# Optimization experiments

Measured on AMD Instinct MI355X. Metric: run time of the kernel, lower is better.

## Reference

```python
import jax, jax.numpy as jnp
import numpy as np

EMBED_DIM = 1024
NUM_HEADS = 16
HEAD_DIM = EMBED_DIM // NUM_HEADS
BSZ, SEQ = 2, 2048


def setup_inputs() -> dict:
    key = jax.random.key(0)
    ks = jax.random.split(key, 7)
    s = 0.02  # keep logits in a sane range
    return {
        "hidden_states": jax.random.normal(ks[0], (BSZ, SEQ, EMBED_DIM), jnp.float32),
        "attention_mask": jnp.zeros((1, 1, SEQ, SEQ), jnp.float32),
        "q_w": jax.random.normal(ks[1], (2 * EMBED_DIM, EMBED_DIM), jnp.float32) * s,
        "q_b": jnp.zeros((2 * EMBED_DIM,), jnp.float32),
        "k_w": jax.random.normal(ks[2], (EMBED_DIM, EMBED_DIM), jnp.float32) * s,
        "k_b": jnp.zeros((EMBED_DIM,), jnp.float32),
        "v_w": jax.random.normal(ks[3], (EMBED_DIM, EMBED_DIM), jnp.float32) * s,
        "v_b": jnp.zeros((EMBED_DIM,), jnp.float32),
        "o_w": jax.random.normal(ks[4], (EMBED_DIM, EMBED_DIM), jnp.float32) * s,
        "o_b": jnp.zeros((EMBED_DIM,), jnp.float32),
    }


def reference(hidden_states, attention_mask, q_w, q_b, k_w, k_b, v_w, v_b, o_w, o_b):
    bsz, seq, _ = hidden_states.shape
    h, d = NUM_HEADS, HEAD_DIM
    inv_sqrt_d = 1.0 / np.sqrt(d).astype(np.float32)

    qg = hidden_states @ q_w.T + q_b                      # [b, s, 2*h*d]
    q, gate_logits = jnp.split(qg, [h * d], axis=-1)       # elementwise gate
    k = hidden_states @ k_w.T + k_b
    v = hidden_states @ v_w.T + v_b

    q = q.reshape(bsz, seq, h, d).transpose(0, 2, 1, 3)    # [b, h, s, d]
    k = k.reshape(bsz, seq, h, d).transpose(0, 2, 1, 3)
    v = v.reshape(bsz, seq, h, d).transpose(0, 2, 1, 3)

    scores = jnp.einsum("bhqd,bhkd->bhqk", q, k) * inv_sqrt_d
    scores = scores + attention_mask
    weights = jax.nn.softmax(scores, axis=-1)
    attn = jnp.einsum("bhqk,bhkd->bhqd", weights, v)       # [b, h, s, d]

    gate = jax.nn.sigmoid(gate_logits.reshape(bsz, seq, h, d).transpose(0, 2, 1, 3))
    attn = attn * gate

    attn = attn.transpose(0, 2, 1, 3).reshape(bsz, seq, h * d)
    return attn @ o_w.T + o_b
```

## Files before the change

### kernel.cpp

```cpp
#include <hip/hip_runtime.h>
#include <cstdint>
#include <cstddef>

#define AS1 __attribute__((address_space(1)))
#define AS3 __attribute__((address_space(3)))

typedef __bf16 bf16x8 __attribute__((ext_vector_type(8)));
typedef __bf16 bf16x4 __attribute__((ext_vector_type(4)));
typedef float  f32x4  __attribute__((ext_vector_type(4)));
typedef float  f32x16 __attribute__((ext_vector_type(16)));
typedef unsigned int u32x4 __attribute__((ext_vector_type(4)));

#define MFMA_BF16(a, b, c) __builtin_amdgcn_mfma_f32_16x16x32_bf16((a), (b), (c), 0, 0, 0)
#define MFMA32(a, b, c)    __builtin_amdgcn_mfma_f32_32x32x16_bf16((a), (b), (c), 0, 0, 0)

__device__ __forceinline__ void gload16(const __bf16* g, __bf16* l) {
  __builtin_amdgcn_global_load_lds((AS1 void*)(uintptr_t)g, (AS3 void*)l, 16, 0, 0);
}

__device__ __forceinline__ unsigned int cvtpk_bf16(float lo, float hi) {
  unsigned int r;
  asm("v_cvt_pk_bf16_f32 %0, %1, %2" : "=v"(r) : "v"(lo), "v"(hi));
  return r;
}

__device__ __forceinline__ void permswap(unsigned int& a, unsigned int& b) {
  asm volatile("v_permlane32_swap_b32 %0, %1" : "+v"(a), "+v"(b));
}

__device__ __forceinline__ float exp2_fast(float x) {
  float r;
  asm("v_exp_f32 %0, %1" : "=v"(r) : "v"(x));
  return r;
}

#define LOG2E 1.4426950408889634f

__global__ void cvt_all_kernel(
    const float* __restrict__ hs, const float* __restrict__ qw, const float* __restrict__ kw,
    const float* __restrict__ vw, const float* __restrict__ ow,
    __bf16* __restrict__ Xb, __bf16* __restrict__ qwb, __bf16* __restrict__ kwb,
    __bf16* __restrict__ vwb, __bf16* __restrict__ owb,
    const unsigned long long* __restrict__ mask, int* __restrict__ flag)
{
  const int gid = blockIdx.x * blockDim.x + threadIdx.x;
  const int stride = gridDim.x * blockDim.x;
  for (int i = gid; i < 1179648; i += stride) {
    const float* s; __bf16* d; int o;
    if (i < 524288)       { s = hs; d = Xb;  o = i; }
    else if (i < 786432)  { s = qw; d = qwb; o = i - 524288; }
    else if (i < 917504)  { s = kw; d = kwb; o = i - 786432; }
    else if (i < 1048576) { s = vw; d = vwb; o = i - 917504; }
    else                  { s = ow; d = owb; o = i - 1048576; }
    const float4* p = (const float4*)(s + (size_t)o * 8);
    float4 a = p[0], b = p[1];
    bf16x8 v;
    v[0] = (__bf16)a.x; v[1] = (__bf16)a.y; v[2] = (__bf16)a.z; v[3] = (__bf16)a.w;
    v[4] = (__bf16)b.x; v[5] = (__bf16)b.y; v[6] = (__bf16)b.z; v[7] = (__bf16)b.w;
    *(bf16x8*)(d + (size_t)o * 8) = v;
  }
  bool nz = false;
  for (int i = gid; i < 2097152; i += stride) nz |= (mask[i] != 0ull);
  if (nz) atomicOr(flag, 1);
}

__global__ __launch_bounds__(256) void proj_kernel(
    const __bf16* __restrict__ X,
    const __bf16* __restrict__ qw, const float* __restrict__ qb,
    const __bf16* __restrict__ kw, const float* __restrict__ kb,
    const __bf16* __restrict__ vw, const float* __restrict__ vb,
    __bf16* __restrict__ Qo, __bf16* __restrict__ Ko,
    __bf16* __restrict__ VTo, __bf16* __restrict__ Go)
{
  __shared__ __bf16 As[2][128][64];
  __shared__ __bf16 Bs[2][128][64];

  const int bid = blockIdx.x;
  const int r = bid >> 3;
  const int ntile = (bid & 7) * 4 + (r >> 5);
  const int mtile = r & 31;
  const int m0 = mtile * 128;
  const int n0 = ntile * 128;

  const __bf16* W; const float* bias; int nb;
  if (n0 < 2048)      { W = qw; bias = qb; nb = n0; }
  else if (n0 < 3072) { W = kw; bias = kb; nb = n0 - 2048; }
  else                { W = vw; bias = vb; nb = n0 - 3072; }

  const int tid = threadIdx.x;
  const int wv = tid >> 6, ln = tid & 63;
  const int wr = wv >> 1, wc = wv & 1;
  const int qr = ln & 15, qg = ln >> 4;
  const int lrow = ln >> 3, lcol = (ln & 7) * 8;

  f32x4 acc[4][4];
#pragma unroll
  for (int m = 0; m < 4; ++m)
#pragma unroll
    for (int n = 0; n < 4; ++n) acc[m][n] = 0.f;

  __bf16 (*Asc)[64] = As[0], (*Asn)[64] = As[1];
  __bf16 (*Bsc)[64] = Bs[0], (*Bsn)[64] = Bs[1];

#pragma unroll
  for (int i = 0; i < 4; ++i) {
    const int rb = i * 32 + wv * 8;
    gload16(X + (size_t)(m0 + rb + lrow) * 1024 + lcol, &Asc[rb][0]);
    gload16(W + (size_t)(nb + rb + lrow) * 1024 + lcol, &Bsc[rb][0]);
  }
  __syncthreads();

  for (int t = 0; t < 16; ++t) {
    if (t < 15) {
      const int k0 = (t + 1) * 64;
#pragma unroll
      for (int i = 0; i < 4; ++i) {
        const int rb = i * 32 + wv * 8;
        gload16(X + (size_t)(m0 + rb + lrow) * 1024 + k0 + lcol, &Asn[rb][0]);
        gload16(W + (size_t)(nb + rb + lrow) * 1024 + k0 + lcol, &Bsn[rb][0]);
      }
    }
#pragma unroll
    for (int kk = 0; kk < 2; ++kk) {
      bf16x8 af[4], bfv[4];
#pragma unroll
      for (int m = 0; m < 4; ++m) af[m] = *(const bf16x8*)&Asc[wr * 64 + m * 16 + qr][kk * 32 + qg * 8];
#pragma unroll
      for (int n = 0; n < 4; ++n) bfv[n] = *(const bf16x8*)&Bsc[wc * 64 + n * 16 + qr][kk * 32 + qg * 8];
#pragma unroll
      for (int m = 0; m < 4; ++m)
#pragma unroll
        for (int n = 0; n < 4; ++n) acc[m][n] = MFMA_BF16(af[m], bfv[n], acc[m][n]);
    }
    __syncthreads();
    __bf16 (*ta)[64] = Asc; Asc = Asn; Asn = ta;
    __bf16 (*tb)[64] = Bsc; Bsc = Bsn; Bsn = tb;
  }

#pragma unroll
  for (int m = 0; m < 4; ++m) {
    const int gm0 = m0 + wr * 64 + m * 16 + qg * 4;
    const int b = gm0 >> 11;
    const int s = gm0 & 2047;
#pragma unroll
    for (int n = 0; n < 4; ++n) {
      const int nl = wc * 64 + n * 16 + qr;
      const float bb = bias[nb + nl];
      if (n0 < 1024) {
        const int col = n0 + nl, hh = col >> 6, dd = col & 63;
        __bf16* dst = Qo + ((size_t)((b << 4) + hh)) * 131072 + (size_t)s * 64 + dd;
#pragma unroll
        for (int rr = 0; rr < 4; ++rr) dst[(size_t)rr * 64] = (__bf16)((acc[m][n][rr] + bb) * (0.125f * LOG2E));
      } else if (n0 < 2048) {
        const int j = n0 - 1024 + nl;
        __bf16* dst = Go + (size_t)gm0 * 1024 + j;
#pragma unroll
        for (int rr = 0; rr < 4; ++rr) {
          const float v = acc[m][n][rr] + bb;
          dst[(size_t)rr * 1024] = (__bf16)(1.f / (1.f + __expf(-v)));
        }
      } else if (n0 < 3072) {
        const int j = n0 - 2048 + nl, hh = j >> 6, dd = j & 63;
        __bf16* dst = Ko + ((size_t)((b << 4) + hh)) * 131072 + (size_t)s * 64 + dd;
#pragma unroll
        for (int rr = 0; rr < 4; ++rr) dst[(size_t)rr * 64] = (__bf16)(acc[m][n][rr] + bb);
      } else {
        const int j = n0 - 3072 + nl, hh = j >> 6, dd = j & 63;
        bf16x4 pv;
#pragma unroll
        for (int rr = 0; rr < 4; ++rr) pv[rr] = (__bf16)(acc[m][n][rr] + bb);
        *(bf16x4*)(VTo + ((size_t)((b << 4) + hh)) * 131072 + (size_t)dd * 2048 + s) = pv;
      }
    }
  }
}

__global__ __launch_bounds__(256, 2) void attn_kernel(
    const __bf16* __restrict__ Qb, const __bf16* __restrict__ Kb,
    const __bf16* __restrict__ VT, const __bf16* __restrict__ G,
    const float* __restrict__ mask, const int* __restrict__ flag,
    __bf16* __restrict__ attn)
{
  __shared__ __bf16 Ksh[2][32][128];
  __shared__ __bf16 Vsh[2][32][128];

  const int bid = blockIdx.x;
  const int y = bid >> 3;
  const int hl = (bid & 7) * 4 + (y >> 4);
  const int tid = threadIdx.x;
  const int w = tid >> 6;
  const int ln = tid & 63;
  const int lq = ln & 31;
  const int hi = ln >> 5;
  const int q0 = (y & 15) * 128 + w * 32;
  const int b = hl >> 4, h = hl & 15;

  const __bf16* Qh = Qb + (size_t)hl * 131072;
  const __bf16* Kh = Kb + (size_t)hl * 131072;
  const __bf16* Vh = VT + (size_t)hl * 131072;

  int kco[2], vco[2], ldst[2];
#pragma unroll
  for (int i = 0; i < 2; ++i) {
    const int prow = w * 8 + i * 4 + (ln >> 4);
    const int bphys = (ln & 15) * 16;
    const int blog = bphys ^ ((prow & 15) << 4);
    const int half = blog >> 7;
    const int col = (blog & 127) >> 1;
    kco[i] = (half * 32 + prow) * 64 + col;
    vco[i] = (half * 32 + prow) * 2048 + col;
    ldst[i] = (w * 8 + i * 4) * 256;
  }
  const int swz = (lq & 15) << 4;
  const int krow = lq * 256;

  bf16x8 qf[4];
#pragma unroll
  for (int ks = 0; ks < 4; ++ks)
    qf[ks] = *(const bf16x8*)(Qh + (size_t)(q0 + lq) * 64 + ks * 16 + hi * 8);

  f32x16 o0, o1;
#pragma unroll
  for (int i = 0; i < 16; ++i) { o0[i] = 0.f; o1[i] = 0.f; }
  float mrun = -1e30f, lrun = 0.f;

  const bool um = (*flag) != 0;

  char* Kc = (char*)&Ksh[0][0][0];  char* Kn = (char*)&Ksh[1][0][0];
  char* Vc = (char*)&Vsh[0][0][0];  char* Vn = (char*)&Vsh[1][0][0];

#pragma unroll
  for (int i = 0; i < 2; ++i) {
    gload16(Kh + kco[i], (__bf16*)(Kc + ldst[i]));
    gload16(Vh + vco[i], (__bf16*)(Vc + ldst[i]));
  }
  __syncthreads();

  for (int c = 0; c < 32; ++c) {
    const int kv0 = c * 64;
    if (c < 31) {
      const int kvn = kv0 + 64;
#pragma unroll
      for (int i = 0; i < 2; ++i) {
        gload16(Kh + kvn * 64 + kco[i], (__bf16*)(Kn + ldst[i]));
        gload16(Vh + kvn + vco[i],      (__bf16*)(Vn + ldst[i]));
      }
    }

#pragma unroll
    for (int s32 = 0; s32 < 2; ++s32) {
      bf16x8 kf[4];
#pragma unroll
      for (int ks = 0; ks < 4; ++ks)
        kf[ks] = *(const bf16x8*)(Kc + krow + ((s32 * 128 + ks * 32 + hi * 16) ^ swz));

      f32x16 s;
#pragma unroll
      for (int i = 0; i < 16; ++i) s[i] = 0.f;
      __builtin_amdgcn_s_setprio(1);
#pragma unroll
      for (int ks = 0; ks < 4; ++ks) s = MFMA32(kf[ks], qf[ks], s);
      __builtin_amdgcn_s_setprio(0);

      float p[16];
      if (um) {
        const size_t mrow = (size_t)(q0 + lq) * 2048 + kv0 + s32 * 32;
#pragma unroll
        for (int i = 0; i < 16; ++i)
          p[i] = s[i] + mask[mrow + (i & 3) + 8 * (i >> 2) + 4 * hi] * LOG2E;
      } else {
#pragma unroll
        for (int i = 0; i < 16; ++i) p[i] = s[i];
      }

      float t = fmaxf(fmaxf(p[0], p[1]), p[2]);
      t = fmaxf(fmaxf(t, p[3]), p[4]);
      t = fmaxf(fmaxf(t, p[5]), p[6]);
      t = fmaxf(fmaxf(t, p[7]), p[8]);
      t = fmaxf(fmaxf(t, p[9]), p[10]);
      t = fmaxf(fmaxf(t, p[11]), p[12]);
      t = fmaxf(fmaxf(t, p[13]), p[14]);
      t = fmaxf(t, p[15]);
      t = fmaxf(t, __shfl_xor(t, 32));

      if (t > mrun + 8.f) {
        const float al = exp2_fast(mrun - t);
        mrun = t;
        lrun *= al;
#pragma unroll
        for (int i = 0; i < 16; ++i) { o0[i] *= al; o1[i] *= al; }
      }

      float ps = 0.f;
#pragma unroll
      for (int i = 0; i < 16; ++i) { p[i] = exp2_fast(p[i] - mrun); ps += p[i]; }
      lrun += ps;

      bf16x8 pa[2];
#pragma unroll
      for (int ks = 0; ks < 2; ++ks) {
        unsigned int c0 = cvtpk_bf16(p[8 * ks + 0], p[8 * ks + 1]);
        unsigned int c1 = cvtpk_bf16(p[8 * ks + 2], p[8 * ks + 3]);
        unsigned int c2 = cvtpk_bf16(p[8 * ks + 4], p[8 * ks + 5]);
        unsigned int c3 = cvtpk_bf16(p[8 * ks + 6], p[8 * ks + 7]);
        permswap(c0, c2);
        permswap(c1, c3);
        u32x4 wv; wv.x = c0; wv.y = c1; wv.z = c2; wv.w = c3;
        pa[ks] = __builtin_bit_cast(bf16x8, wv);
      }

      __builtin_amdgcn_s_setprio(1);
#pragma unroll
      for (int ks = 0; ks < 2; ++ks) {
        const int kvb = s32 * 64 + ks * 32 + hi * 16;
        bf16x8 v0 = *(const bf16x8*)(Vc + krow + ((0 + kvb) ^ swz));
        bf16x8 v1 = *(const bf16x8*)(Vc + krow + ((128 + kvb) ^ swz));
        o0 = MFMA32(v0, pa[ks], o0);
        o1 = MFMA32(v1, pa[ks], o1);
      }
      __builtin_amdgcn_s_setprio(0);
    }
    __syncthreads();
    char* tk = Kc; Kc = Kn; Kn = tk;
    char* tv = Vc; Vc = Vn; Vn = tv;
  }

  lrun += __shfl_xor(lrun, 32);
  const float inv = 1.f / lrun;
  const size_t base = ((size_t)(b * 2048 + q0 + lq)) * 1024 + h * 64;
#pragma unroll
  for (int half = 0; half < 2; ++half) {
#pragma unroll
    for (int g = 0; g < 4; ++g) {
      const int d0 = half * 32 + g * 8 + hi * 4;
      bf16x4 g4 = *(const bf16x4*)(G + base + d0);
      bf16x4 r4;
#pragma unroll
      for (int j = 0; j < 4; ++j) {
        const float ov = half ? o1[g * 4 + j] : o0[g * 4 + j];
        r4[j] = (__bf16)(ov * inv * (float)g4[j]);
      }
      *(bf16x4*)(attn + base + d0) = r4;
    }
  }
}

__global__ __launch_bounds__(256) void oproj_kernel(
    const __bf16* __restrict__ A, const __bf16* __restrict__ ow,
    const float* __restrict__ ob, float* __restrict__ C)
{
  __shared__ __bf16 As[2][128][64];
  __shared__ __bf16 Bs[2][128][64];
  const int bid = blockIdx.x;
  const int ntile = bid & 7;
  const int mtile = bid >> 3;
  const int m0 = mtile * 128, n0 = ntile * 128;

  const int tid = threadIdx.x;
  const int wv = tid >> 6, ln = tid & 63;
  const int wr = wv >> 1, wc = wv & 1;
  const int qr = ln & 15, qg = ln >> 4;
  const int lrow = ln >> 3, lcol = (ln & 7) * 8;

  f32x4 acc[4][4];
#pragma unroll
  for (int m = 0; m < 4; ++m)
#pragma unroll
    for (int n = 0; n < 4; ++n) acc[m][n] = 0.f;

  __bf16 (*Asc)[64] = As[0], (*Asn)[64] = As[1];
  __bf16 (*Bsc)[64] = Bs[0], (*Bsn)[64] = Bs[1];

#pragma unroll
  for (int i = 0; i < 4; ++i) {
    const int rb = i * 32 + wv * 8;
    gload16(A  + (size_t)(m0 + rb + lrow) * 1024 + lcol, &Asc[rb][0]);
    gload16(ow + (size_t)(n0 + rb + lrow) * 1024 + lcol, &Bsc[rb][0]);
  }
  __syncthreads();

  for (int t = 0; t < 16; ++t) {
    if (t < 15) {
      const int k0 = (t + 1) * 64;
#pragma unroll
      for (int i = 0; i < 4; ++i) {
        const int rb = i * 32 + wv * 8;
        gload16(A  + (size_t)(m0 + rb + lrow) * 1024 + k0 + lcol, &Asn[rb][0]);
        gload16(ow + (size_t)(n0 + rb + lrow) * 1024 + k0 + lcol, &Bsn[rb][0]);
      }
    }
#pragma unroll
    for (int kk = 0; kk < 2; ++kk) {
      bf16x8 af[4], bfv[4];
#pragma unroll
      for (int m = 0; m < 4; ++m) af[m] = *(const bf16x8*)&Asc[wr * 64 + m * 16 + qr][kk * 32 + qg * 8];
#pragma unroll
      for (int n = 0; n < 4; ++n) bfv[n] = *(const bf16x8*)&Bsc[wc * 64 + n * 16 + qr][kk * 32 + qg * 8];
#pragma unroll
      for (int m = 0; m < 4; ++m)
#pragma unroll
        for (int n = 0; n < 4; ++n) acc[m][n] = MFMA_BF16(af[m], bfv[n], acc[m][n]);
    }
    __syncthreads();
    __bf16 (*ta)[64] = Asc; Asc = Asn; Asn = ta;
    __bf16 (*tb)[64] = Bsc; Bsc = Bsn; Bsn = tb;
  }

#pragma unroll
  for (int m = 0; m < 4; ++m) {
    const int gm0 = m0 + wr * 64 + m * 16 + qg * 4;
#pragma unroll
    for (int n = 0; n < 4; ++n) {
      const int gn = n0 + wc * 64 + n * 16 + qr;
      const float bb = ob[gn];
      float* dst = C + (size_t)gm0 * 1024 + gn;
#pragma unroll
      for (int rr = 0; rr < 4; ++rr) dst[(size_t)rr * 1024] = acc[m][n][rr] + bb;
    }
  }
}

extern "C" void kernel_launch(void* const* d_in, const int* in_sizes, int n_in,
                              void* d_out, int out_size, void* d_ws, size_t ws_size,
                              hipStream_t stream)
{
  const float* hs   = (const float*)d_in[0];
  const float* mask = (const float*)d_in[1];
  const float* qw   = (const float*)d_in[2];
  const float* qb   = (const float*)d_in[3];
  const float* kw   = (const float*)d_in[4];
  const float* kb   = (const float*)d_in[5];
  const float* vw   = (const float*)d_in[6];
  const float* vb   = (const float*)d_in[7];
  const float* ow   = (const float*)d_in[8];
  const float* ob   = (const float*)d_in[9];
  float* out = (float*)d_out;

  char* w = (char*)d_ws;
  int*    flag = (int*)w;
  __bf16* Xb  = (__bf16*)(w + 256);
  __bf16* qwb = Xb  + 4194304;
  __bf16* kwb = qwb + 2097152;
  __bf16* vwb = kwb + 1048576;
  __bf16* owb = vwb + 1048576;
  __bf16* Qo  = owb + 1048576;
  __bf16* Ko  = Qo  + 4194304;
  __bf16* VTo = Ko  + 4194304;
  __bf16* Go  = VTo + 4194304;
  __bf16* At  = Go  + 4194304;

  hipMemsetAsync(flag, 0, sizeof(int), stream);
  cvt_all_kernel<<<2048, 256, 0, stream>>>(hs, qw, kw, vw, ow, Xb, qwb, kwb, vwb, owb,
                                           (const unsigned long long*)mask, flag);
  proj_kernel<<<1024, 256, 0, stream>>>(Xb, qwb, qb, kwb, kb, vwb, vb, Qo, Ko, VTo, Go);
  attn_kernel<<<512, 256, 0, stream>>>(Qo, Ko, VTo, Go, mask, flag, At);
  oproj_kernel<<<256, 256, 0, stream>>>(At, owb, ob, out);
}
```

Baseline: 150.0 us.

## Split attention KV range across warp pairs with in-block softmax merge

The attention kernel now gives each block 64 queries instead of 128 and splits the KV sequence into two halves. Each pair of waves processes one half, and the partial outputs and max/sum statistics are merged through shared memory at the end (a split-K flash-decoding style combine). This doubles the grid to 1024 blocks, raises the occupancy hint to 4, and removes the K/V double-buffer prefetch in favour of a single buffer per half, so loads are no longer overlapped with compute. The projection kernel's tile mapping is also reordered so that n-tiles vary fastest.

After: 153.7 us. 1.02x slower.

```diff
diff --git a/kernel.cpp b/kernel.cpp
--- a/kernel.cpp
+++ b/kernel.cpp
@@ -77,8 +77,8 @@
 
   const int bid = blockIdx.x;
   const int r = bid >> 3;
-  const int ntile = (bid & 7) * 4 + (r >> 5);
-  const int mtile = r & 31;
+  const int ntile = (bid & 7) * 4 + (r & 3);
+  const int mtile = r >> 2;
   const int m0 = mtile * 128;
   const int n0 = ntile * 128;
 
@@ -175,49 +175,56 @@
   }
 }
 
-__global__ __launch_bounds__(256, 2) void attn_kernel(
+__global__ __launch_bounds__(256, 4) void attn_kernel(
     const __bf16* __restrict__ Qb, const __bf16* __restrict__ Kb,
     const __bf16* __restrict__ VT, const __bf16* __restrict__ G,
     const float* __restrict__ mask, const int* __restrict__ flag,
     __bf16* __restrict__ attn)
 {
-  __shared__ __bf16 Ksh[2][32][128];
-  __shared__ __bf16 Vsh[2][32][128];
+  __shared__ __bf16 KVsh[2][2][32][128];
+  __shared__ float ML0[2][64], ML1[2][64];
 
   const int bid = blockIdx.x;
   const int y = bid >> 3;
-  const int hl = (bid & 7) * 4 + (y >> 4);
+  const int hl = (bid & 7) * 4 + (y >> 5);
+  const int q0 = (y & 31) * 64;
   const int tid = threadIdx.x;
   const int w = tid >> 6;
+  const int qsub = w & 1;
+  const int halfsel = w >> 1;
   const int ln = tid & 63;
   const int lq = ln & 31;
   const int hi = ln >> 5;
-  const int q0 = (y & 15) * 128 + w * 32;
+  const int qg0 = q0 + qsub * 32;
   const int b = hl >> 4, h = hl & 15;
 
   const __bf16* Qh = Qb + (size_t)hl * 131072;
-  const __bf16* Kh = Kb + (size_t)hl * 131072;
-  const __bf16* Vh = VT + (size_t)hl * 131072;
-
-  int kco[2], vco[2], ldst[2];
-#pragma unroll
-  for (int i = 0; i < 2; ++i) {
-    const int prow = w * 8 + i * 4 + (ln >> 4);
+  const __bf16* Kh = Kb + (size_t)hl * 131072 + halfsel * 1024 * 64;
+  const __bf16* Vh = VT + (size_t)hl * 131072 + halfsel * 1024;
+
+  const int wi = qsub;
+  int kco[4], vco[4], ldst[4];
+#pragma unroll
+  for (int i = 0; i < 4; ++i) {
+    const int prow = wi * 16 + i * 4 + (ln >> 4);
     const int bphys = (ln & 15) * 16;
     const int blog = bphys ^ ((prow & 15) << 4);
-    const int half = blog >> 7;
+    const int sub = blog >> 7;
     const int col = (blog & 127) >> 1;
-    kco[i] = (half * 32 + prow) * 64 + col;
-    vco[i] = (half * 32 + prow) * 2048 + col;
-    ldst[i] = (w * 8 + i * 4) * 256;
+    kco[i] = (sub * 32 + prow) * 64 + col;
+    vco[i] = (sub * 32 + prow) * 2048 + col;
+    ldst[i] = (wi * 16 + i * 4) * 256;
   }
   const int swz = (lq & 15) << 4;
   const int krow = lq * 256;
 
+  char* Kc = (char*)&KVsh[0][halfsel][0][0];
+  char* Vc = (char*)&KVsh[1][halfsel][0][0];
+
   bf16x8 qf[4];
 #pragma unroll
   for (int ks = 0; ks < 4; ++ks)
-    qf[ks] = *(const bf16x8*)(Qh + (size_t)(q0 + lq) * 64 + ks * 16 + hi * 8);
+    qf[ks] = *(const bf16x8*)(Qh + (size_t)(qg0 + lq) * 64 + ks * 16 + hi * 8);
 
   f32x16 o0, o1;
 #pragma unroll
@@ -226,26 +233,14 @@
 
   const bool um = (*flag) != 0;
 
-  char* Kc = (char*)&Ksh[0][0][0];  char* Kn = (char*)&Ksh[1][0][0];
-  char* Vc = (char*)&Vsh[0][0][0];  char* Vn = (char*)&Vsh[1][0][0];
-
-#pragma unroll
-  for (int i = 0; i < 2; ++i) {
-    gload16(Kh + kco[i], (__bf16*)(Kc + ldst[i]));
-    gload16(Vh + vco[i], (__bf16*)(Vc + ldst[i]));
-  }
-  __syncthreads();
-
-  for (int c = 0; c < 32; ++c) {
+  for (int c = 0; c < 16; ++c) {
     const int kv0 = c * 64;
-    if (c < 31) {
-      const int kvn = kv0 + 64;
-#pragma unroll
-      for (int i = 0; i < 2; ++i) {
-        gload16(Kh + kvn * 64 + kco[i], (__bf16*)(Kn + ldst[i]));
-        gload16(Vh + kvn + vco[i],      (__bf16*)(Vn + ldst[i]));
-      }
-    }
+#pragma unroll
+    for (int i = 0; i < 4; ++i) {
+      gload16(Kh + kv0 * 64 + kco[i], (__bf16*)(Kc + ldst[i]));
+      gload16(Vh + kv0 + vco[i],      (__bf16*)(Vc + ldst[i]));
+    }
+    __syncthreads();
 
 #pragma unroll
     for (int s32 = 0; s32 < 2; ++s32) {
@@ -264,7 +259,7 @@
 
       float p[16];
       if (um) {
-        const size_t mrow = (size_t)(q0 + lq) * 2048 + kv0 + s32 * 32;
+        const size_t mrow = (size_t)(qg0 + lq) * 2048 + halfsel * 1024 + kv0 + s32 * 32;
 #pragma unroll
         for (int i = 0; i < 16; ++i)
           p[i] = s[i] + mask[mrow + (i & 3) + 8 * (i >> 2) + 4 * hi] * LOG2E;
@@ -305,8 +300,8 @@
         unsigned int c3 = cvtpk_bf16(p[8 * ks + 6], p[8 * ks + 7]);
         permswap(c0, c2);
         permswap(c1, c3);
-        u32x4 wv; wv.x = c0; wv.y = c1; wv.z = c2; wv.w = c3;
-        pa[ks] = __builtin_bit_cast(bf16x8, wv);
+        u32x4 wvv; wvv.x = c0; wvv.y = c1; wvv.z = c2; wvv.w = c3;
+        pa[ks] = __builtin_bit_cast(bf16x8, wvv);
       }
 
       __builtin_amdgcn_s_setprio(1);
@@ -321,27 +316,45 @@
       __builtin_amdgcn_s_setprio(0);
     }
     __syncthreads();
-    char* tk = Kc; Kc = Kn; Kn = tk;
-    char* tv = Vc; Vc = Vn; Vn = tv;
   }
 
   lrun += __shfl_xor(lrun, 32);
-  const float inv = 1.f / lrun;
-  const size_t base = ((size_t)(b * 2048 + q0 + lq)) * 1024 + h * 64;
-#pragma unroll
-  for (int half = 0; half < 2; ++half) {
-#pragma unroll
-    for (int g = 0; g < 4; ++g) {
-      const int d0 = half * 32 + g * 8 + hi * 4;
-      bf16x4 g4 = *(const bf16x4*)(G + base + d0);
-      bf16x4 r4;
-#pragma unroll
-      for (int j = 0; j < 4; ++j) {
-        const float ov = half ? o1[g * 4 + j] : o0[g * 4 + j];
-        r4[j] = (__bf16)(ov * inv * (float)g4[j]);
-      }
-      *(bf16x4*)(attn + base + d0) = r4;
-    }
+  float* Obuf = (float*)&KVsh[0][0][0][0];
+#pragma unroll
+  for (int r = 0; r < 16; ++r) {
+    const int d0 = (r & 3) + 8 * (r >> 2) + 4 * hi;
+    Obuf[halfsel * 4096 + d0 * 64 + qsub * 32 + lq] = o0[r];
+    Obuf[halfsel * 4096 + (d0 + 32) * 64 + qsub * 32 + lq] = o1[r];
+  }
+  if (hi == 0) { ML0[halfsel][qsub * 32 + lq] = mrun; ML1[halfsel][qsub * 32 + lq] = lrun; }
+  __syncthreads();
+
+  {
+    const int cq = tid & 63;
+    const int seg = tid >> 6;
+    const float m0 = ML0[0][cq], m1 = ML0[1][cq];
+    const float M = fmaxf(m0, m1);
+    const float e0 = exp2_fast(m0 - M), e1 = exp2_fast(m1 - M);
+    const float L = e0 * ML1[0][cq] + e1 * ML1[1][cq];
+    const float inv = 1.f / L;
+    const size_t base = ((size_t)(b * 2048 + q0 + cq)) * 1024 + h * 64 + seg * 16;
+    bf16x8 g0 = *(const bf16x8*)(G + base);
+    bf16x8 g1 = *(const bf16x8*)(G + base + 8);
+    bf16x8 r0, r1;
+#pragma unroll
+    for (int j = 0; j < 8; ++j) {
+      const int d = seg * 16 + j;
+      const float sacc = e0 * Obuf[d * 64 + cq] + e1 * Obuf[4096 + d * 64 + cq];
+      r0[j] = (__bf16)(sacc * inv * (float)g0[j]);
+    }
+#pragma unroll
+    for (int j = 0; j < 8; ++j) {
+      const int d = seg * 16 + 8 + j;
+      const float sacc = e0 * Obuf[d * 64 + cq] + e1 * Obuf[4096 + d * 64 + cq];
+      r1[j] = (__bf16)(sacc * inv * (float)g1[j]);
+    }
+    *(bf16x8*)(attn + base) = r0;
+    *(bf16x8*)(attn + base + 8) = r1;
   }
 }
 
@@ -453,6 +466,6 @@
   cvt_all_kernel<<<2048, 256, 0, stream>>>(hs, qw, kw, vw, ow, Xb, qwb, kwb, vwb, owb,
                                            (const unsigned long long*)mask, flag);
   proj_kernel<<<1024, 256, 0, stream>>>(Xb, qwb, qb, kwb, kb, vwb, vb, Qo, Ko, VTo, Go);
-  attn_kernel<<<512, 256, 0, stream>>>(Qo, Ko, VTo, Go, mask, flag, At);
+  attn_kernel<<<1024, 256, 0, stream>>>(Qo, Ko, VTo, Go, mask, flag, At);
   oproj_kernel<<<256, 256, 0, stream>>>(At, owb, ob, out);
 }
```

## Rewrite QKV projection GEMM with 256x256 tiles, swizzled LDS and interleaved pipeline

Applied to the files above, without the earlier changes.

The QKV projection kernel moves from 128x128 tiles with 256 threads to 256x256 tiles with 512 threads. It uses 128KB of dynamic shared memory with XOR-swizzled layouts to avoid bank conflicts. The main loop is software-pipelined in half-tiles: global-to-LDS loads are interleaved with quadrant MFMA blocks under fine-grained barriers, explicit vmcnt waits and setprio. The aim is higher data reuse per tile and better load/compute overlap. The cost is more registers, more barriers, only 256 blocks on the device, and 128KB of LDS per block, which limits occupancy.

New measurement: 137.2 us. -8.6%, faster.

```diff
diff --git a/kernel.cpp b/kernel.cpp
--- a/kernel.cpp
+++ b/kernel.cpp
@@ -64,7 +64,7 @@
   if (nz) atomicOr(flag, 1);
 }
 
-__global__ __launch_bounds__(256) void proj_kernel(
+__global__ __launch_bounds__(512, 2) void proj_kernel(
     const __bf16* __restrict__ X,
     const __bf16* __restrict__ qw, const float* __restrict__ qb,
     const __bf16* __restrict__ kw, const float* __restrict__ kb,
@@ -72,15 +72,13 @@
     __bf16* __restrict__ Qo, __bf16* __restrict__ Ko,
     __bf16* __restrict__ VTo, __bf16* __restrict__ Go)
 {
-  __shared__ __bf16 As[2][128][64];
-  __shared__ __bf16 Bs[2][128][64];
+  extern __shared__ char smem[];
 
   const int bid = blockIdx.x;
-  const int r = bid >> 3;
-  const int ntile = (bid & 7) * 4 + (r >> 5);
-  const int mtile = r & 31;
-  const int m0 = mtile * 128;
-  const int n0 = ntile * 128;
+  const int jj = bid >> 3;
+  const int ntile = (bid & 7) * 2 + (jj >> 4);
+  const int mtile = jj & 15;
+  const int m0 = mtile * 256, n0 = ntile * 256;
 
   const __bf16* W; const float* bias; int nb;
   if (n0 < 2048)      { W = qw; bias = qb; nb = n0; }
@@ -88,91 +86,162 @@
   else                { W = vw; bias = vb; nb = n0 - 3072; }
 
   const int tid = threadIdx.x;
-  const int wv = tid >> 6, ln = tid & 63;
-  const int wr = wv >> 1, wc = wv & 1;
+  const int wid = tid >> 6;
+  const int wr = wid >> 2;
+  const int wc = wid & 3;
+  const int ln = tid & 63;
   const int qr = ln & 15, qg = ln >> 4;
-  const int lrow = ln >> 3, lcol = (ln & 7) * 8;
-
-  f32x4 acc[4][4];
-#pragma unroll
-  for (int m = 0; m < 4; ++m)
+
+  const int srow = ln >> 3;
+  const int sgran = ((ln & 7) ^ srow) * 8;
+
+#define SA(buf, half, kt) do { \
+  _Pragma("unroll") for (int i_ = 0; i_ < 2; ++i_) { \
+    const int r0_ = (half) * 64 + i_ * 128 + wid * 8; \
+    gload16(X + (size_t)(m0 + r0_ + srow) * 1024 + (kt) * 64 + sgran, \
+            (__bf16*)(smem + (buf) * 32768 + r0_ * 128)); \
+  } } while (0)
+
+#define SB(buf, half, kt) do { \
+  _Pragma("unroll") for (int i_ = 0; i_ < 2; ++i_) { \
+    const int g_ = wid + i_ * 8; \
+    const int r0_ = (g_ >> 2) * 64 + (half) * 32 + (g_ & 3) * 8; \
+    gload16(W + (size_t)(nb + r0_ + srow) * 1024 + (kt) * 64 + sgran, \
+            (__bf16*)(smem + 65536 + (buf) * 32768 + r0_ * 128)); \
+  } } while (0)
+
+#define LDA(buf, mh, mi, kk) (*(const bf16x8*)(smem + (buf) * 32768 + \
+    (wr * 128 + (mh) * 64 + (mi) * 16 + qr) * 128 + (((kk) * 64 + qg * 16) ^ ((qr & 7) << 4))))
+#define LDB(buf, nh, ni, kk) (*(const bf16x8*)(smem + 65536 + (buf) * 32768 + \
+    (wc * 64 + (nh) * 32 + (ni) * 16 + qr) * 128 + (((kk) * 64 + qg * 16) ^ ((qr & 7) << 4))))
+
+  f32x4 acc[8][4];
+#pragma unroll
+  for (int m = 0; m < 8; ++m)
 #pragma unroll
     for (int n = 0; n < 4; ++n) acc[m][n] = 0.f;
 
-  __bf16 (*Asc)[64] = As[0], (*Asn)[64] = As[1];
-  __bf16 (*Bsc)[64] = Bs[0], (*Bsn)[64] = Bs[1];
-
-#pragma unroll
-  for (int i = 0; i < 4; ++i) {
-    const int rb = i * 32 + wv * 8;
-    gload16(X + (size_t)(m0 + rb + lrow) * 1024 + lcol, &Asc[rb][0]);
-    gload16(W + (size_t)(nb + rb + lrow) * 1024 + lcol, &Bsc[rb][0]);
-  }
-  __syncthreads();
-
-  for (int t = 0; t < 16; ++t) {
-    if (t < 15) {
-      const int k0 = (t + 1) * 64;
-#pragma unroll
-      for (int i = 0; i < 4; ++i) {
-        const int rb = i * 32 + wv * 8;
-        gload16(X + (size_t)(m0 + rb + lrow) * 1024 + k0 + lcol, &Asn[rb][0]);
-        gload16(W + (size_t)(nb + rb + lrow) * 1024 + k0 + lcol, &Bsn[rb][0]);
-      }
-    }
-#pragma unroll
-    for (int kk = 0; kk < 2; ++kk) {
-      bf16x8 af[4], bfv[4];
-#pragma unroll
-      for (int m = 0; m < 4; ++m) af[m] = *(const bf16x8*)&Asc[wr * 64 + m * 16 + qr][kk * 32 + qg * 8];
-#pragma unroll
-      for (int n = 0; n < 4; ++n) bfv[n] = *(const bf16x8*)&Bsc[wc * 64 + n * 16 + qr][kk * 32 + qg * 8];
-#pragma unroll
-      for (int m = 0; m < 4; ++m)
-#pragma unroll
-        for (int n = 0; n < 4; ++n) acc[m][n] = MFMA_BF16(af[m], bfv[n], acc[m][n]);
-    }
-    __syncthreads();
-    __bf16 (*ta)[64] = Asc; Asc = Asn; Asn = ta;
-    __bf16 (*tb)[64] = Bsc; Bsc = Bsn; Bsn = tb;
-  }
-
-#pragma unroll
-  for (int m = 0; m < 4; ++m) {
-    const int gm0 = m0 + wr * 64 + m * 16 + qg * 4;
+  bf16x8 af[4][2], b0f[2][2], b1f[2][2];
+
+#define QUAD(mh, nh, BF) do { \
+  asm volatile("s_waitcnt lgkmcnt(0)"); \
+  __builtin_amdgcn_sched_barrier(0); \
+  __builtin_amdgcn_s_setprio(1); \
+  _Pragma("unroll") for (int mi_ = 0; mi_ < 4; ++mi_) \
+    _Pragma("unroll") for (int ni_ = 0; ni_ < 2; ++ni_) { \
+      acc[(mh)*4+mi_][(nh)*2+ni_] = MFMA_BF16(af[mi_][0], BF[ni_][0], acc[(mh)*4+mi_][(nh)*2+ni_]); \
+      acc[(mh)*4+mi_][(nh)*2+ni_] = MFMA_BF16(af[mi_][1], BF[ni_][1], acc[(mh)*4+mi_][(nh)*2+ni_]); \
+    } \
+  __builtin_amdgcn_s_setprio(0); \
+} while (0)
+
+#define BAR() __builtin_amdgcn_s_barrier()
+
+  SA(0, 0, 0); SA(0, 1, 0); SB(0, 0, 0); SB(0, 1, 0);
+  SA(1, 0, 1); SB(1, 0, 1); SB(1, 1, 1);
+  asm volatile("s_waitcnt vmcnt(6)");
+  BAR();
+
+  for (int it = 0; it < 8; ++it) {
+    const int tb = 2 * it + 1;
+    const int tc = (2 * it + 2 < 16) ? 2 * it + 2 : 15;
+    const int td = (2 * it + 3 < 16) ? 2 * it + 3 : 15;
+
+#pragma unroll
+    for (int mi = 0; mi < 4; ++mi) { af[mi][0] = LDA(0, 0, mi, 0); af[mi][1] = LDA(0, 0, mi, 1); }
+#pragma unroll
+    for (int ni = 0; ni < 2; ++ni) { b0f[ni][0] = LDB(0, 0, ni, 0); b0f[ni][1] = LDB(0, 0, ni, 1); }
+    SA(1, 1, tb);
+    BAR();
+    QUAD(0, 0, b0f);
+    BAR();
+#pragma unroll
+    for (int ni = 0; ni < 2; ++ni) { b1f[ni][0] = LDB(0, 1, ni, 0); b1f[ni][1] = LDB(0, 1, ni, 1); }
+    SA(0, 0, tc);
+    BAR();
+    QUAD(0, 1, b1f);
+    BAR();
+#pragma unroll
+    for (int mi = 0; mi < 4; ++mi) { af[mi][0] = LDA(0, 1, mi, 0); af[mi][1] = LDA(0, 1, mi, 1); }
+    SB(0, 0, tc);
+    BAR();
+    QUAD(1, 1, b1f);
+    BAR();
+    SB(0, 1, tc);
+    asm volatile("s_waitcnt vmcnt(6)");
+    BAR();
+    QUAD(1, 0, b0f);
+    BAR();
+
+#pragma unroll
+    for (int mi = 0; mi < 4; ++mi) { af[mi][0] = LDA(1, 0, mi, 0); af[mi][1] = LDA(1, 0, mi, 1); }
+#pragma unroll
+    for (int ni = 0; ni < 2; ++ni) { b0f[ni][0] = LDB(1, 0, ni, 0); b0f[ni][1] = LDB(1, 0, ni, 1); }
+    SA(0, 1, tc);
+    BAR();
+    QUAD(0, 0, b0f);
+    BAR();
+#pragma unroll
+    for (int ni = 0; ni < 2; ++ni) { b1f[ni][0] = LDB(1, 1, ni, 0); b1f[ni][1] = LDB(1, 1, ni, 1); }
+    SA(1, 0, td);
+    BAR();
+    QUAD(0, 1, b1f);
+    BAR();
+#pragma unroll
+    for (int mi = 0; mi < 4; ++mi) { af[mi][0] = LDA(1, 1, mi, 0); af[mi][1] = LDA(1, 1, mi, 1); }
+    SB(1, 0, td);
+    BAR();
+    QUAD(1, 1, b1f);
+    BAR();
+    SB(1, 1, td);
+    asm volatile("s_waitcnt vmcnt(6)");
+    BAR();
+    QUAD(1, 0, b0f);
+    BAR();
+  }
+
+#pragma unroll
+  for (int mi = 0; mi < 8; ++mi) {
+    const int gm0 = m0 + wr * 128 + mi * 16 + qg * 4;
     const int b = gm0 >> 11;
     const int s = gm0 & 2047;
 #pragma unroll
-    for (int n = 0; n < 4; ++n) {
-      const int nl = wc * 64 + n * 16 + qr;
+    for (int ni = 0; ni < 4; ++ni) {
+      const int nl = wc * 64 + ni * 16 + qr;
       const float bb = bias[nb + nl];
       if (n0 < 1024) {
         const int col = n0 + nl, hh = col >> 6, dd = col & 63;
         __bf16* dst = Qo + ((size_t)((b << 4) + hh)) * 131072 + (size_t)s * 64 + dd;
 #pragma unroll
-        for (int rr = 0; rr < 4; ++rr) dst[(size_t)rr * 64] = (__bf16)((acc[m][n][rr] + bb) * (0.125f * LOG2E));
+        for (int rr = 0; rr < 4; ++rr) dst[(size_t)rr * 64] = (__bf16)((acc[mi][ni][rr] + bb) * (0.125f * LOG2E));
       } else if (n0 < 2048) {
         const int j = n0 - 1024 + nl;
         __bf16* dst = Go + (size_t)gm0 * 1024 + j;
 #pragma unroll
         for (int rr = 0; rr < 4; ++rr) {
-          const float v = acc[m][n][rr] + bb;
+          const float v = acc[mi][ni][rr] + bb;
           dst[(size_t)rr * 1024] = (__bf16)(1.f / (1.f + __expf(-v)));
         }
       } else if (n0 < 3072) {
         const int j = n0 - 2048 + nl, hh = j >> 6, dd = j & 63;
         __bf16* dst = Ko + ((size_t)((b << 4) + hh)) * 131072 + (size_t)s * 64 + dd;
 #pragma unroll
-        for (int rr = 0; rr < 4; ++rr) dst[(size_t)rr * 64] = (__bf16)(acc[m][n][rr] + bb);
+        for (int rr = 0; rr < 4; ++rr) dst[(size_t)rr * 64] = (__bf16)(acc[mi][ni][rr] + bb);
       } else {
         const int j = n0 - 3072 + nl, hh = j >> 6, dd = j & 63;
         bf16x4 pv;
 #pragma unroll
-        for (int rr = 0; rr < 4; ++rr) pv[rr] = (__bf16)(acc[m][n][rr] + bb);
+        for (int rr = 0; rr < 4; ++rr) pv[rr] = (__bf16)(acc[mi][ni][rr] + bb);
         *(bf16x4*)(VTo + ((size_t)((b << 4) + hh)) * 131072 + (size_t)dd * 2048 + s) = pv;
       }
     }
   }
+#undef SA
+#undef SB
+#undef LDA
+#undef LDB
+#undef QUAD
+#undef BAR
 }
 
 __global__ __launch_bounds__(256, 2) void attn_kernel(
@@ -449,10 +518,12 @@
   __bf16* Go  = VTo + 4194304;
   __bf16* At  = Go  + 4194304;
 
+  hipFuncSetAttribute((const void*)proj_kernel, hipFuncAttributeMaxDynamicSharedMemorySize, 131072);
+
   hipMemsetAsync(flag, 0, sizeof(int), stream);
   cvt_all_kernel<<<2048, 256, 0, stream>>>(hs, qw, kw, vw, ow, Xb, qwb, kwb, vwb, owb,
                                            (const unsigned long long*)mask, flag);
-  proj_kernel<<<1024, 256, 0, stream>>>(Xb, qwb, qb, kwb, kb, vwb, vb, Qo, Ko, VTo, Go);
+  proj_kernel<<<256, 512, 131072, stream>>>(Xb, qwb, qb, kwb, kb, vwb, vb, Qo, Ko, VTo, Go);
   attn_kernel<<<512, 256, 0, stream>>>(Qo, Ko, VTo, Go, mask, flag, At);
   oproj_kernel<<<256, 256, 0, stream>>>(At, owb, ob, out);
 }
```
